# Optimization experiments

Measured on AMD Instinct MI355X. Metric: run time of the kernel, lower is better.

## Reference

```python
import jax, jax.numpy as jnp
import numpy as np

N, M = 1024, 1024
GATES = ["ii", "hi", "if", "hf", "ig", "hg", "io", "ho"]


def setup_inputs() -> dict:
    key = jax.random.key(0)
    names = ["x", "h", "c"] + [f"{p}_{g}" for g in GATES for p in ("L", "R", "b")]
    keys = jax.random.split(key, len(names))
    out = {}
    for nm, k in zip(names, keys):
        if nm in ("x", "h", "c"):
            sh = (N, M)
            scale = 1.0
        else:
            p = nm.split("_")[0]
            sh = {"L": (N, N), "R": (M, M), "b": (N, M)}[p]
            scale = 0.05  # keep gate pre-activations in a sane range
        out[nm] = jax.random.normal(k, sh, dtype=jnp.float32) * scale
    return out


def _klin(L, R, b, x):
    # kronecker_addmm: left @ x @ right + bias
    return L @ x @ R + b


def reference(x, h, c,
              L_ii, R_ii, b_ii, L_hi, R_hi, b_hi,
              L_if, R_if, b_if, L_hf, R_hf, b_hf,
              L_ig, R_ig, b_ig, L_hg, R_hg, b_hg,
              L_io, R_io, b_io, L_ho, R_ho, b_ho):
    i = jax.nn.sigmoid(_klin(L_ii, R_ii, b_ii, x) + _klin(L_hi, R_hi, b_hi, h))
    f = jax.nn.sigmoid(_klin(L_if, R_if, b_if, x) + _klin(L_hf, R_hf, b_hf, h))
    g = jnp.tanh(_klin(L_ig, R_ig, b_ig, x) + _klin(L_hg, R_hg, b_hg, h))
    o = jax.nn.sigmoid(_klin(L_io, R_io, b_io, x) + _klin(L_ho, R_ho, b_ho, h))
    c_new = f * c + i * g
    h_new = o * jnp.tanh(c_new)
    return (h_new, c_new)
```

## Files before the change

kernel.cpp:

```cpp
#include <hip/hip_runtime.h>
#include <stdint.h>

typedef __bf16 bf16x8 __attribute__((ext_vector_type(8)));
typedef float  f32x4  __attribute__((ext_vector_type(4)));
typedef uint16_t u16;

#define MAT_ELEMS (1024 * 1024)
#define LDK 1024


__device__ __forceinline__ u16 to_bf16(float f) {
  union { float f; uint32_t u; } v; v.f = f;
  uint32_t u = v.u;
  uint32_t r = u + 0x7FFFu + ((u >> 16) & 1u);
  return (u16)(r >> 16);
}

__device__ __forceinline__ float bf16_to_f32(u16 b) {
  union { uint32_t u; float f; } v; v.u = ((uint32_t)b) << 16;
  return v.f;
}

__device__ __forceinline__ void gll16(const void* g, void* l) {
  __builtin_amdgcn_global_load_lds(
      (__attribute__((address_space(1))) void*)const_cast<void*>(g),
      (__attribute__((address_space(3))) void*)(l),
      16, 0, 0);
}

__device__ __forceinline__ float fast_sigmoid(float x) {
  x = fminf(fmaxf(x, -30.f), 30.f);
  return 1.0f / (1.0f + __expf(-x));
}

__device__ __forceinline__ float fast_tanh(float x) {
  x = fminf(fmaxf(x, -15.f), 15.f);
  float e = __expf(2.0f * x);
  return (e - 1.0f) / (e + 1.0f);
}


struct P8  { const float* p[8]; };
struct P10 { const float* p[10]; };
struct B8  { const float* b[8]; };

__global__ __launch_bounds__(256) void cast8_kernel(P8 s, u16* __restrict__ dst) {
  const float* src = s.p[blockIdx.y];
  u16* d = dst + ((size_t)blockIdx.y << 20);
  int i = (blockIdx.x * 256 + threadIdx.x) * 4;
  f32x4 v = *reinterpret_cast<const f32x4*>(src + i);
  ushort4 o;
  o.x = to_bf16(v[0]); o.y = to_bf16(v[1]);
  o.z = to_bf16(v[2]); o.w = to_bf16(v[3]);
  *reinterpret_cast<ushort4*>(d + i) = o;
}

__global__ __launch_bounds__(256) void transpose_cast_kernel(P10 s, u16* __restrict__ dstbase) {
  __shared__ float tile[32][65];
  const float* src = s.p[blockIdx.z];
  u16* dst = dstbase + ((size_t)blockIdx.z << 20);
  int c0 = blockIdx.x * 64;
  int r0 = blockIdx.y * 32;
  int cl = threadIdx.x & 63;
  int rg = threadIdx.x >> 6;
#pragma unroll
  for (int i = 0; i < 8; ++i) {
    int r = rg + i * 4;
    tile[r][cl] = src[(size_t)(r0 + r) * 1024 + c0 + cl];
  }
  __syncthreads();
  int kl = threadIdx.x & 31;
  int ng = threadIdx.x >> 5;
#pragma unroll
  for (int i = 0; i < 8; ++i) {
    int n = ng + i * 8;
    dst[(size_t)(c0 + n) * 1024 + r0 + kl] = to_bf16(tile[kl][n]);
  }
}


__device__ __forceinline__ void gemm128_dbuf(
    const u16* __restrict__ A, const u16* __restrict__ B,
    int row0, int col0, u16* __restrict__ out,
    u16* As0, u16* As1, u16* Bs0, u16* Bs1)
{
  const int tid  = threadIdx.x;
  const int lane = tid & 63;
  const int w    = tid >> 6;
  const int wr   = w >> 1;
  const int wc   = w & 1;
  const int r16  = lane & 15;
  const int kg   = lane >> 4;

  f32x4 acc[4][4];
#pragma unroll
  for (int m = 0; m < 4; ++m)
#pragma unroll
    for (int n = 0; n < 4; ++n) {
      f32x4 z = {0.f, 0.f, 0.f, 0.f};
      acc[m][n] = z;
    }

  const int srow = tid >> 2;
  const int skk  = (tid & 3) * 8;

  auto stage = [&](u16* Asb, u16* Bsb, int kt) {
    const u16* Ak = A + kt * 32 + skk;
    const u16* Bk = B + kt * 32 + skk;
    gll16(Ak + (size_t)(row0 + srow)      * LDK, Asb + srow * 32 + skk);
    gll16(Ak + (size_t)(row0 + srow + 64) * LDK, Asb + (srow + 64) * 32 + skk);
    gll16(Bk + (size_t)(col0 + srow)      * LDK, Bsb + srow * 32 + skk);
    gll16(Bk + (size_t)(col0 + srow + 64) * LDK, Bsb + (srow + 64) * 32 + skk);
  };

  auto compute = [&](const u16* Asb, const u16* Bsb) {
    bf16x8 af[4], bfr[4];
#pragma unroll
    for (int m = 0; m < 4; ++m)
      af[m] = *reinterpret_cast<const bf16x8*>(Asb + (wr * 64 + m * 16 + r16) * 32 + kg * 8);
#pragma unroll
    for (int n = 0; n < 4; ++n)
      bfr[n] = *reinterpret_cast<const bf16x8*>(Bsb + (wc * 64 + n * 16 + r16) * 32 + kg * 8);
#pragma unroll
    for (int m = 0; m < 4; ++m)
#pragma unroll
      for (int n = 0; n < 4; ++n)
        acc[m][n] = __builtin_amdgcn_mfma_f32_16x16x32_bf16(af[m], bfr[n], acc[m][n], 0, 0, 0);
  };

  stage(As0, Bs0, 0);
  __syncthreads();

  for (int kt = 0; kt < 32; kt += 2) {
    stage(As1, Bs1, kt + 1);
    compute(As0, Bs0);
    __syncthreads();
    if (kt + 2 < 32) stage(As0, Bs0, kt + 2);
    compute(As1, Bs1);
    __syncthreads();
  }

#pragma unroll
  for (int m = 0; m < 4; ++m) {
#pragma unroll
    for (int r = 0; r < 4; ++r) {
      int row = row0 + wr * 64 + m * 16 + kg * 4 + r;
#pragma unroll
      for (int n = 0; n < 4; ++n) {
        int col = col0 + wc * 64 + n * 16 + r16;
        out[(size_t)row * 1024 + col] = to_bf16(acc[m][n][r]);
      }
    }
  }
}

__device__ __forceinline__ void swz_decode(int bx, int& g, int& row0, int& col0) {
  int wg = ((bx & 7) << 6) | (bx >> 3);
  g = wg >> 6;
  int tile = wg & 63;
  row0 = (tile >> 3) * 128;
  col0 = (tile & 7) * 128;
}

__global__ __launch_bounds__(256) void gemm_stage1_kernel(
    const u16* __restrict__ Lb, const u16* __restrict__ xT,
    const u16* __restrict__ hT, u16* __restrict__ Tbuf)
{
  __shared__ u16 As0[128 * 32], As1[128 * 32];
  __shared__ u16 Bs0[128 * 32], Bs1[128 * 32];
  int g, row0, col0;
  swz_decode(blockIdx.x, g, row0, col0);
  const u16* A = Lb + ((size_t)g << 20);
  const u16* B = (g & 1) ? hT : xT;
  gemm128_dbuf(A, B, row0, col0, Tbuf + ((size_t)g << 20), As0, As1, Bs0, Bs1);
}

__global__ __launch_bounds__(256) void gemm_stage2_kernel(
    const u16* __restrict__ Tbuf, const u16* __restrict__ RT,
    u16* __restrict__ P)
{
  __shared__ u16 As0[128 * 32], As1[128 * 32];
  __shared__ u16 Bs0[128 * 32], Bs1[128 * 32];
  int g, row0, col0;
  swz_decode(blockIdx.x, g, row0, col0);
  const u16* A = Tbuf + ((size_t)g << 20);
  const u16* B = RT   + ((size_t)g << 20);
  gemm128_dbuf(A, B, row0, col0, P + ((size_t)g << 20), As0, As1, Bs0, Bs1);
}

__global__ __launch_bounds__(256) void lstm_cell_kernel(
    const u16* __restrict__ P, B8 bp, const float* __restrict__ c,
    float* __restrict__ out)
{
  int i = (blockIdx.x * 256 + threadIdx.x) * 4;
  ushort4 pv[8];
#pragma unroll
  for (int g = 0; g < 8; ++g)
    pv[g] = *reinterpret_cast<const ushort4*>(P + (size_t)g * MAT_ELEMS + i);
  f32x4 bv[8];
#pragma unroll
  for (int g = 0; g < 8; ++g)
    bv[g] = *reinterpret_cast<const f32x4*>(bp.b[g] + i);
  f32x4 cc = *reinterpret_cast<const f32x4*>(c + i);
  f32x4 hn, cn;
#pragma unroll
  for (int j = 0; j < 4; ++j) {
    float pi = bf16_to_f32((&pv[0].x)[j]) + bf16_to_f32((&pv[1].x)[j]) + bv[0][j] + bv[1][j];
    float pf = bf16_to_f32((&pv[2].x)[j]) + bf16_to_f32((&pv[3].x)[j]) + bv[2][j] + bv[3][j];
    float pg = bf16_to_f32((&pv[4].x)[j]) + bf16_to_f32((&pv[5].x)[j]) + bv[4][j] + bv[5][j];
    float po = bf16_to_f32((&pv[6].x)[j]) + bf16_to_f32((&pv[7].x)[j]) + bv[6][j] + bv[7][j];
    float ig = fast_sigmoid(pi);
    float fg = fast_sigmoid(pf);
    float gg = fast_tanh(pg);
    float og = fast_sigmoid(po);
    float cv = fg * cc[j] + ig * gg;
    cn[j] = cv;
    hn[j] = og * fast_tanh(cv);
  }
  *reinterpret_cast<f32x4*>(out + i) = hn;
  *reinterpret_cast<f32x4*>(out + MAT_ELEMS + i) = cn;
}


extern "C" void kernel_launch(void* const* d_in, const int* in_sizes, int n_in,
                              void* d_out, int out_size, void* d_ws, size_t ws_size,
                              hipStream_t stream) {
  const float* x = (const float*)d_in[0];
  const float* h = (const float*)d_in[1];
  const float* c = (const float*)d_in[2];

  u16* Lb   = (u16*)d_ws;
  u16* xT   = Lb + ((size_t)8 << 20);
  u16* hT   = xT + ((size_t)1 << 20);
  u16* RT   = hT + ((size_t)1 << 20);
  u16* Tbuf = RT + ((size_t)8 << 20);
  u16* P    = Tbuf + ((size_t)8 << 20);

  P8 lp;
  for (int g = 0; g < 8; ++g) lp.p[g] = (const float*)d_in[3 + 3 * g];
  P10 tp;
  tp.p[0] = x; tp.p[1] = h;
  for (int g = 0; g < 8; ++g) tp.p[2 + g] = (const float*)d_in[4 + 3 * g];
  B8 bp;
  for (int g = 0; g < 8; ++g) bp.b[g] = (const float*)d_in[5 + 3 * g];

  cast8_kernel<<<dim3(1024, 8), 256, 0, stream>>>(lp, Lb);
  transpose_cast_kernel<<<dim3(16, 32, 10), 256, 0, stream>>>(tp, xT);
  gemm_stage1_kernel<<<512, 256, 0, stream>>>(Lb, xT, hT, Tbuf);
  gemm_stage2_kernel<<<512, 256, 0, stream>>>(Tbuf, RT, P);
  lstm_cell_kernel<<<1024, 256, 0, stream>>>(P, bp, c, (float*)d_out);
}
```

Baseline: 232.2 us.

## Use 128x256 GEMM tiles with 8 waves, swizzled LDS and explicit vmcnt barriers

Both bf16 GEMM stages move from 128x128 tiles with 4 waves to 128x256 tiles with 8 waves (2x4 wave grid). The grid drops to 256 blocks, so each block reuses its A tile across twice as many output columns. LDS staging now XOR-swizzles the 16-byte k-chunks by row, which is meant to reduce bank conflicts on the fragment reads. __syncthreads is replaced by an explicit vmcnt(0) wait, an s_barrier and a sched_barrier, so the async global-to-LDS loads are known to be complete before the buffer is read. The trade-off is roughly one block per CU with fewer independent workgroups to hide latency, and a larger LDS footprint per block.

```diff
diff --git a/kernel.cpp b/kernel.cpp
--- a/kernel.cpp
+++ b/kernel.cpp
@@ -26,6 +26,12 @@
       (__attribute__((address_space(1))) void*)const_cast<void*>(g),
       (__attribute__((address_space(3))) void*)(l),
       16, 0, 0);
+}
+
+__device__ __forceinline__ void wait_barrier() {
+  asm volatile("s_waitcnt vmcnt(0)" ::: "memory");
+  __builtin_amdgcn_s_barrier();
+  __builtin_amdgcn_sched_barrier(0);
 }
 
 __device__ __forceinline__ float fast_sigmoid(float x) {
@@ -79,18 +85,57 @@
 }
 
 
-__device__ __forceinline__ void gemm128_dbuf(
+struct GemmCtx {
+  const u16* A; const u16* B;
+  int row0, col0;
+  int tid, wr, wc, r16, kg, sw;
+};
+
+__device__ __forceinline__ void stage_tile(const GemmCtx& c, u16* As, u16* Bs, int kt) {
+  int rho = c.tid >> 2;
+  int sig = c.tid & 3;
+  int swc = (sig ^ ((c.tid >> 3) & 3)) * 8;
+  int kcol = kt * 32 + swc;
+  gll16(c.A + (size_t)(c.row0 + rho) * LDK + kcol, As + c.tid * 8);
+  gll16(c.B + (size_t)(c.col0 + rho) * LDK + kcol, Bs + c.tid * 8);
+  gll16(c.B + (size_t)(c.col0 + rho + 128) * LDK + kcol, Bs + c.tid * 8 + 4096);
+}
+
+__device__ __forceinline__ void compute_tile(const GemmCtx& c, const u16* As,
+                                             const u16* Bs, f32x4 acc[4][4]) {
+  bf16x8 af[4], bfr[4];
+#pragma unroll
+  for (int n = 0; n < 4; ++n) {
+    int Rb = c.wc * 64 + n * 16 + c.r16;
+    bfr[n] = *reinterpret_cast<const bf16x8*>(Bs + Rb * 32 + ((c.kg ^ c.sw) * 8));
+  }
+#pragma unroll
+  for (int m = 0; m < 4; ++m) {
+    int Ra = c.wr * 64 + m * 16 + c.r16;
+    af[m] = *reinterpret_cast<const bf16x8*>(As + Ra * 32 + ((c.kg ^ c.sw) * 8));
+  }
+#pragma unroll
+  for (int m = 0; m < 4; ++m)
+#pragma unroll
+    for (int n = 0; n < 4; ++n)
+      acc[m][n] = __builtin_amdgcn_mfma_f32_16x16x32_bf16(af[m], bfr[n], acc[m][n], 0, 0, 0);
+}
+
+__device__ __forceinline__ void gemm_body(
     const u16* __restrict__ A, const u16* __restrict__ B,
     int row0, int col0, u16* __restrict__ out,
-    u16* As0, u16* As1, u16* Bs0, u16* Bs1)
-{
-  const int tid  = threadIdx.x;
-  const int lane = tid & 63;
-  const int w    = tid >> 6;
-  const int wr   = w >> 1;
-  const int wc   = w & 1;
-  const int r16  = lane & 15;
-  const int kg   = lane >> 4;
+    u16* As0, u16* Bs0, u16* As1, u16* Bs1)
+{
+  GemmCtx c;
+  c.A = A; c.B = B; c.row0 = row0; c.col0 = col0;
+  c.tid = threadIdx.x;
+  int lane = c.tid & 63;
+  int w = c.tid >> 6;
+  c.wr  = w >> 2;
+  c.wc  = w & 3;
+  c.r16 = lane & 15;
+  c.kg  = lane >> 4;
+  c.sw  = (c.r16 >> 1) & 3;
 
   f32x4 acc[4][4];
 #pragma unroll
@@ -101,53 +146,26 @@
       acc[m][n] = z;
     }
 
-  const int srow = tid >> 2;
-  const int skk  = (tid & 3) * 8;
-
-  auto stage = [&](u16* Asb, u16* Bsb, int kt) {
-    const u16* Ak = A + kt * 32 + skk;
-    const u16* Bk = B + kt * 32 + skk;
-    gll16(Ak + (size_t)(row0 + srow)      * LDK, Asb + srow * 32 + skk);
-    gll16(Ak + (size_t)(row0 + srow + 64) * LDK, Asb + (srow + 64) * 32 + skk);
-    gll16(Bk + (size_t)(col0 + srow)      * LDK, Bsb + srow * 32 + skk);
-    gll16(Bk + (size_t)(col0 + srow + 64) * LDK, Bsb + (srow + 64) * 32 + skk);
-  };
-
-  auto compute = [&](const u16* Asb, const u16* Bsb) {
-    bf16x8 af[4], bfr[4];
-#pragma unroll
-    for (int m = 0; m < 4; ++m)
-      af[m] = *reinterpret_cast<const bf16x8*>(Asb + (wr * 64 + m * 16 + r16) * 32 + kg * 8);
-#pragma unroll
-    for (int n = 0; n < 4; ++n)
-      bfr[n] = *reinterpret_cast<const bf16x8*>(Bsb + (wc * 64 + n * 16 + r16) * 32 + kg * 8);
-#pragma unroll
-    for (int m = 0; m < 4; ++m)
-#pragma unroll
-      for (int n = 0; n < 4; ++n)
-        acc[m][n] = __builtin_amdgcn_mfma_f32_16x16x32_bf16(af[m], bfr[n], acc[m][n], 0, 0, 0);
-  };
-
-  stage(As0, Bs0, 0);
-  __syncthreads();
+  stage_tile(c, As0, Bs0, 0);
+  wait_barrier();
 
   for (int kt = 0; kt < 32; kt += 2) {
-    stage(As1, Bs1, kt + 1);
-    compute(As0, Bs0);
-    __syncthreads();
-    if (kt + 2 < 32) stage(As0, Bs0, kt + 2);
-    compute(As1, Bs1);
-    __syncthreads();
+    stage_tile(c, As1, Bs1, kt + 1);
+    compute_tile(c, As0, Bs0, acc);
+    wait_barrier();
+    if (kt + 2 < 32) stage_tile(c, As0, Bs0, kt + 2);
+    compute_tile(c, As1, Bs1, acc);
+    wait_barrier();
   }
 
 #pragma unroll
   for (int m = 0; m < 4; ++m) {
 #pragma unroll
     for (int r = 0; r < 4; ++r) {
-      int row = row0 + wr * 64 + m * 16 + kg * 4 + r;
+      int row = row0 + c.wr * 64 + m * 16 + c.kg * 4 + r;
 #pragma unroll
       for (int n = 0; n < 4; ++n) {
-        int col = col0 + wc * 64 + n * 16 + r16;
+        int col = col0 + c.wc * 64 + n * 16 + c.r16;
         out[(size_t)row * 1024 + col] = to_bf16(acc[m][n][r]);
       }
     }
@@ -155,37 +173,37 @@
 }
 
 __device__ __forceinline__ void swz_decode(int bx, int& g, int& row0, int& col0) {
-  int wg = ((bx & 7) << 6) | (bx >> 3);
-  g = wg >> 6;
-  int tile = wg & 63;
-  row0 = (tile >> 3) * 128;
-  col0 = (tile & 7) * 128;
-}
-
-__global__ __launch_bounds__(256) void gemm_stage1_kernel(
+  int wg = ((bx & 7) << 5) | (bx >> 3);
+  g = wg >> 5;
+  int t = wg & 31;
+  row0 = (t >> 2) * 128;
+  col0 = (t & 3) * 256;
+}
+
+__global__ __launch_bounds__(512) void gemm_stage1_kernel(
     const u16* __restrict__ Lb, const u16* __restrict__ xT,
     const u16* __restrict__ hT, u16* __restrict__ Tbuf)
 {
-  __shared__ u16 As0[128 * 32], As1[128 * 32];
-  __shared__ u16 Bs0[128 * 32], Bs1[128 * 32];
+  __shared__ u16 As0[128 * 32], Bs0[256 * 32];
+  __shared__ u16 As1[128 * 32], Bs1[256 * 32];
   int g, row0, col0;
   swz_decode(blockIdx.x, g, row0, col0);
   const u16* A = Lb + ((size_t)g << 20);
   const u16* B = (g & 1) ? hT : xT;
-  gemm128_dbuf(A, B, row0, col0, Tbuf + ((size_t)g << 20), As0, As1, Bs0, Bs1);
-}
-
-__global__ __launch_bounds__(256) void gemm_stage2_kernel(
+  gemm_body(A, B, row0, col0, Tbuf + ((size_t)g << 20), As0, Bs0, As1, Bs1);
+}
+
+__global__ __launch_bounds__(512) void gemm_stage2_kernel(
     const u16* __restrict__ Tbuf, const u16* __restrict__ RT,
     u16* __restrict__ P)
 {
-  __shared__ u16 As0[128 * 32], As1[128 * 32];
-  __shared__ u16 Bs0[128 * 32], Bs1[128 * 32];
+  __shared__ u16 As0[128 * 32], Bs0[256 * 32];
+  __shared__ u16 As1[128 * 32], Bs1[256 * 32];
   int g, row0, col0;
   swz_decode(blockIdx.x, g, row0, col0);
   const u16* A = Tbuf + ((size_t)g << 20);
   const u16* B = RT   + ((size_t)g << 20);
-  gemm128_dbuf(A, B, row0, col0, P + ((size_t)g << 20), As0, As1, Bs0, Bs1);
+  gemm_body(A, B, row0, col0, P + ((size_t)g << 20), As0, Bs0, As1, Bs1);
 }
 
 __global__ __launch_bounds__(256) void lstm_cell_kernel(
@@ -246,7 +264,7 @@
 
   cast8_kernel<<<dim3(1024, 8), 256, 0, stream>>>(lp, Lb);
   transpose_cast_kernel<<<dim3(16, 32, 10), 256, 0, stream>>>(tp, xT);
-  gemm_stage1_kernel<<<512, 256, 0, stream>>>(Lb, xT, hT, Tbuf);
-  gemm_stage2_kernel<<<512, 256, 0, stream>>>(Tbuf, RT, P);
+  gemm_stage1_kernel<<<256, 512, 0, stream>>>(Lb, xT, hT, Tbuf);
+  gemm_stage2_kernel<<<256, 512, 0, stream>>>(Tbuf, RT, P);
   lstm_cell_kernel<<<1024, 256, 0, stream>>>(P, bp, c, (float*)d_out);
 }
```

Result: slower. 242.3 us (+4.4%).

## Replace 128x128 GEMM with 256x256 eight-wave pipelined tile kernel

Applied to the files above, without the earlier changes.

The two batched GEMM stages move from 128x128 tiles (256 threads, BK=32) to 256x256 tiles with 512 threads, BK=64 and 128 KB of dynamic LDS. The new kernel uses an XOR-swizzled LDS layout and splits each k-tile into four phases that interleave global-to-LDS loads with MFMA bursts under explicit barriers, s_setprio and vmcnt waits. The aim is more data reuse per tile, fewer LDS bank conflicts and loads overlapped with compute. The cost is only 128 workgroups on a 256-CU device, so about half the CUs sit idle, plus high register and LDS pressure.

```diff
diff --git a/kernel.cpp b/kernel.cpp
--- a/kernel.cpp
+++ b/kernel.cpp
@@ -6,7 +6,6 @@
 typedef uint16_t u16;
 
 #define MAT_ELEMS (1024 * 1024)
-#define LDK 1024
 
 
 __device__ __forceinline__ u16 to_bf16(float f) {
@@ -26,6 +25,11 @@
       (__attribute__((address_space(1))) void*)const_cast<void*>(g),
       (__attribute__((address_space(3))) void*)(l),
       16, 0, 0);
+}
+
+__device__ __forceinline__ void barrier_pin() {
+  __builtin_amdgcn_s_barrier();
+  __builtin_amdgcn_sched_barrier(0);
 }
 
 __device__ __forceinline__ float fast_sigmoid(float x) {
@@ -79,113 +83,204 @@
 }
 
 
-__device__ __forceinline__ void gemm128_dbuf(
-    const u16* __restrict__ A, const u16* __restrict__ B,
-    int row0, int col0, u16* __restrict__ out,
-    u16* As0, u16* As1, u16* Bs0, u16* Bs1)
+#define HALF_U16 8192
+#define BUF_U16  16384
+
+__device__ __forceinline__ void stage_half(const u16* __restrict__ src,
+                                           u16* __restrict__ dst, int tid) {
+#pragma unroll
+  for (int s = 0; s < 2; ++s) {
+    int idx = s * 512 + tid;
+    int row = idx >> 3;
+    int gs  = (idx & 7) ^ (row & 7);
+    gll16(src + (size_t)row * 1024 + gs * 8, dst + idx * 8);
+  }
+}
+
+__device__ void gemm8p(const u16* __restrict__ A, const u16* __restrict__ B,
+                       int row0, int col0, u16* __restrict__ out, u16* smem)
 {
   const int tid  = threadIdx.x;
   const int lane = tid & 63;
   const int w    = tid >> 6;
-  const int wr   = w >> 1;
-  const int wc   = w & 1;
+  const int wm   = w >> 2;
+  const int wn   = w & 3;
+  const int wh   = wn >> 1;
   const int r16  = lane & 15;
   const int kg   = lane >> 4;
-
-  f32x4 acc[4][4];
-#pragma unroll
-  for (int m = 0; m < 4; ++m)
+  const int rsw  = r16 & 7;
+  const int brow = (wn & 1) * 64;
+
+  u16* Abuf = smem;
+  u16* Bbuf = smem + 2 * BUF_U16;
+
+  u16* A0w = Abuf + wm * HALF_U16;
+  u16* A1w = Abuf + BUF_U16 + wm * HALF_U16;
+  u16* B0w = Bbuf + wh * HALF_U16;
+  u16* B1w = Bbuf + BUF_U16 + wh * HALF_U16;
+
+  u16* A0d0 = Abuf;            u16* A0d1 = Abuf + HALF_U16;
+  u16* A1d0 = Abuf + BUF_U16;  u16* A1d1 = Abuf + BUF_U16 + HALF_U16;
+  u16* B0d0 = Bbuf;            u16* B0d1 = Bbuf + HALF_U16;
+  u16* B1d0 = Bbuf + BUF_U16;  u16* B1d1 = Bbuf + BUF_U16 + HALF_U16;
+
+  auto asrc = [&](int kt, int h) { return A + (size_t)(row0 + h * 128) * 1024 + kt * 64; };
+  auto bsrc = [&](int kt, int h) { return B + (size_t)(col0 + h * 128) * 1024 + kt * 64; };
+
+  f32x4 acc[8][4];
+#pragma unroll
+  for (int m = 0; m < 8; ++m)
 #pragma unroll
     for (int n = 0; n < 4; ++n) {
       f32x4 z = {0.f, 0.f, 0.f, 0.f};
       acc[m][n] = z;
     }
 
-  const int srow = tid >> 2;
-  const int skk  = (tid & 3) * 8;
-
-  auto stage = [&](u16* Asb, u16* Bsb, int kt) {
-    const u16* Ak = A + kt * 32 + skk;
-    const u16* Bk = B + kt * 32 + skk;
-    gll16(Ak + (size_t)(row0 + srow)      * LDK, Asb + srow * 32 + skk);
-    gll16(Ak + (size_t)(row0 + srow + 64) * LDK, Asb + (srow + 64) * 32 + skk);
-    gll16(Bk + (size_t)(col0 + srow)      * LDK, Bsb + srow * 32 + skk);
-    gll16(Bk + (size_t)(col0 + srow + 64) * LDK, Bsb + (srow + 64) * 32 + skk);
+  stage_half(asrc(0, 0), A0d0, tid); stage_half(asrc(0, 1), A0d1, tid);
+  stage_half(bsrc(0, 0), B0d0, tid); stage_half(bsrc(0, 1), B0d1, tid);
+  stage_half(bsrc(1, 0), B1d0, tid); stage_half(bsrc(1, 1), B1d1, tid);
+  asm volatile("s_waitcnt vmcnt(4)" ::: "memory");
+  barrier_pin();
+
+  auto rf = [&](const u16* hb, int rowin, int ks) {
+    int slot = (ks * 4 + kg) ^ rsw;
+    return *reinterpret_cast<const bf16x8*>(hb + rowin * 64 + slot * 8);
   };
 
-  auto compute = [&](const u16* Asb, const u16* Bsb) {
-    bf16x8 af[4], bfr[4];
-#pragma unroll
-    for (int m = 0; m < 4; ++m)
-      af[m] = *reinterpret_cast<const bf16x8*>(Asb + (wr * 64 + m * 16 + r16) * 32 + kg * 8);
-#pragma unroll
-    for (int n = 0; n < 4; ++n)
-      bfr[n] = *reinterpret_cast<const bf16x8*>(Bsb + (wc * 64 + n * 16 + r16) * 32 + kg * 8);
-#pragma unroll
-    for (int m = 0; m < 4; ++m)
-#pragma unroll
-      for (int n = 0; n < 4; ++n)
-        acc[m][n] = __builtin_amdgcn_mfma_f32_16x16x32_bf16(af[m], bfr[n], acc[m][n], 0, 0, 0);
+  auto tile = [&](const u16* Ac, const u16* Bc,
+                  u16* Ad0, u16* Ad1, u16* Bd0, u16* Bd1,
+                  const u16* As0, const u16* As1,
+                  const u16* Bs0, const u16* Bs1,
+                  bool g1, bool g2, bool vm4)
+  {
+    bf16x8 aq[4][2], b01[2][2], b23[2][2];
+#pragma unroll
+    for (int mf = 0; mf < 4; ++mf) {
+      aq[mf][0] = rf(Ac, mf * 16 + r16, 0);
+      aq[mf][1] = rf(Ac, mf * 16 + r16, 1);
+    }
+#pragma unroll
+    for (int nf = 0; nf < 2; ++nf) {
+      b01[nf][0] = rf(Bc, brow + nf * 16 + r16, 0);
+      b01[nf][1] = rf(Bc, brow + nf * 16 + r16, 1);
+    }
+    if (g1) stage_half(As0, Ad0, tid);
+    barrier_pin();
+    __builtin_amdgcn_s_setprio(1);
+#pragma unroll
+    for (int mf = 0; mf < 4; ++mf)
+#pragma unroll
+      for (int nf = 0; nf < 2; ++nf)
+#pragma unroll
+        for (int ks = 0; ks < 2; ++ks)
+          acc[mf][nf] = __builtin_amdgcn_mfma_f32_16x16x32_bf16(aq[mf][ks], b01[nf][ks], acc[mf][nf], 0, 0, 0);
+    __builtin_amdgcn_s_setprio(0);
+    barrier_pin();
+#pragma unroll
+    for (int nf = 0; nf < 2; ++nf) {
+      b23[nf][0] = rf(Bc, brow + (nf + 2) * 16 + r16, 0);
+      b23[nf][1] = rf(Bc, brow + (nf + 2) * 16 + r16, 1);
+    }
+    if (g1) stage_half(As1, Ad1, tid);
+    barrier_pin();
+    __builtin_amdgcn_s_setprio(1);
+#pragma unroll
+    for (int mf = 0; mf < 4; ++mf)
+#pragma unroll
+      for (int nf = 0; nf < 2; ++nf)
+#pragma unroll
+        for (int ks = 0; ks < 2; ++ks)
+          acc[mf][2 + nf] = __builtin_amdgcn_mfma_f32_16x16x32_bf16(aq[mf][ks], b23[nf][ks], acc[mf][2 + nf], 0, 0, 0);
+    __builtin_amdgcn_s_setprio(0);
+    barrier_pin();
+#pragma unroll
+    for (int mf = 0; mf < 4; ++mf) {
+      aq[mf][0] = rf(Ac, 64 + mf * 16 + r16, 0);
+      aq[mf][1] = rf(Ac, 64 + mf * 16 + r16, 1);
+    }
+    if (g2) stage_half(Bs0, Bd0, tid);
+    barrier_pin();
+    __builtin_amdgcn_s_setprio(1);
+#pragma unroll
+    for (int mf = 0; mf < 4; ++mf)
+#pragma unroll
+      for (int nf = 0; nf < 2; ++nf)
+#pragma unroll
+        for (int ks = 0; ks < 2; ++ks)
+          acc[4 + mf][nf] = __builtin_amdgcn_mfma_f32_16x16x32_bf16(aq[mf][ks], b01[nf][ks], acc[4 + mf][nf], 0, 0, 0);
+    __builtin_amdgcn_s_setprio(0);
+    barrier_pin();
+    if (g2) stage_half(Bs1, Bd1, tid);
+    if (vm4) asm volatile("s_waitcnt vmcnt(4)" ::: "memory");
+    else     asm volatile("s_waitcnt vmcnt(0)" ::: "memory");
+    barrier_pin();
+    __builtin_amdgcn_s_setprio(1);
+#pragma unroll
+    for (int mf = 0; mf < 4; ++mf)
+#pragma unroll
+      for (int nf = 0; nf < 2; ++nf)
+#pragma unroll
+        for (int ks = 0; ks < 2; ++ks)
+          acc[4 + mf][2 + nf] = __builtin_amdgcn_mfma_f32_16x16x32_bf16(aq[mf][ks], b23[nf][ks], acc[4 + mf][2 + nf], 0, 0, 0);
+    __builtin_amdgcn_s_setprio(0);
+    barrier_pin();
   };
 
-  stage(As0, Bs0, 0);
-  __syncthreads();
-
-  for (int kt = 0; kt < 32; kt += 2) {
-    stage(As1, Bs1, kt + 1);
-    compute(As0, Bs0);
-    __syncthreads();
-    if (kt + 2 < 32) stage(As0, Bs0, kt + 2);
-    compute(As1, Bs1);
-    __syncthreads();
-  }
-
-#pragma unroll
-  for (int m = 0; m < 4; ++m) {
+  for (int i = 0; i < 8; ++i) {
+    int kt = 2 * i;
+    bool nl = (i < 7);
+    tile(A0w, B0w, A1d0, A1d1, B0d0, B0d1,
+         asrc(kt + 1, 0), asrc(kt + 1, 1), bsrc(kt + 2, 0), bsrc(kt + 2, 1),
+         true, nl, nl);
+    tile(A1w, B1w, A0d0, A0d1, B1d0, B1d1,
+         asrc(kt + 2, 0), asrc(kt + 2, 1), bsrc(kt + 3, 0), bsrc(kt + 3, 1),
+         nl, nl, nl);
+  }
+
+#pragma unroll
+  for (int mf = 0; mf < 8; ++mf) {
 #pragma unroll
     for (int r = 0; r < 4; ++r) {
-      int row = row0 + wr * 64 + m * 16 + kg * 4 + r;
-#pragma unroll
-      for (int n = 0; n < 4; ++n) {
-        int col = col0 + wc * 64 + n * 16 + r16;
-        out[(size_t)row * 1024 + col] = to_bf16(acc[m][n][r]);
+      int row = row0 + wm * 128 + mf * 16 + kg * 4 + r;
+#pragma unroll
+      for (int nf = 0; nf < 4; ++nf) {
+        int col = col0 + wn * 64 + nf * 16 + r16;
+        out[(size_t)row * 1024 + col] = to_bf16(acc[mf][nf][r]);
       }
     }
   }
 }
 
 __device__ __forceinline__ void swz_decode(int bx, int& g, int& row0, int& col0) {
-  int wg = ((bx & 7) << 6) | (bx >> 3);
-  g = wg >> 6;
-  int tile = wg & 63;
-  row0 = (tile >> 3) * 128;
-  col0 = (tile & 7) * 128;
-}
-
-__global__ __launch_bounds__(256) void gemm_stage1_kernel(
+  int wg = ((bx & 7) << 4) | (bx >> 3);
+  g = wg >> 4;
+  int t = wg & 15;
+  row0 = (t >> 2) * 256;
+  col0 = (t & 3) * 256;
+}
+
+__global__ __launch_bounds__(512, 2) void gemm_stage1_kernel(
     const u16* __restrict__ Lb, const u16* __restrict__ xT,
     const u16* __restrict__ hT, u16* __restrict__ Tbuf)
 {
-  __shared__ u16 As0[128 * 32], As1[128 * 32];
-  __shared__ u16 Bs0[128 * 32], Bs1[128 * 32];
+  extern __shared__ u16 smem[];
   int g, row0, col0;
   swz_decode(blockIdx.x, g, row0, col0);
   const u16* A = Lb + ((size_t)g << 20);
   const u16* B = (g & 1) ? hT : xT;
-  gemm128_dbuf(A, B, row0, col0, Tbuf + ((size_t)g << 20), As0, As1, Bs0, Bs1);
-}
-
-__global__ __launch_bounds__(256) void gemm_stage2_kernel(
+  gemm8p(A, B, row0, col0, Tbuf + ((size_t)g << 20), smem);
+}
+
+__global__ __launch_bounds__(512, 2) void gemm_stage2_kernel(
     const u16* __restrict__ Tbuf, const u16* __restrict__ RT,
     u16* __restrict__ P)
 {
-  __shared__ u16 As0[128 * 32], As1[128 * 32];
-  __shared__ u16 Bs0[128 * 32], Bs1[128 * 32];
+  extern __shared__ u16 smem[];
   int g, row0, col0;
   swz_decode(blockIdx.x, g, row0, col0);
   const u16* A = Tbuf + ((size_t)g << 20);
-  const u16* B = RT   + ((size_t)g << 20);
-  gemm128_dbuf(A, B, row0, col0, P + ((size_t)g << 20), As0, As1, Bs0, Bs1);
+  const u16* B = RT + ((size_t)g << 20);
+  gemm8p(A, B, row0, col0, P + ((size_t)g << 20), smem);
 }
 
 __global__ __launch_bounds__(256) void lstm_cell_kernel(
@@ -246,7 +341,7 @@
 
   cast8_kernel<<<dim3(1024, 8), 256, 0, stream>>>(lp, Lb);
   transpose_cast_kernel<<<dim3(16, 32, 10), 256, 0, stream>>>(tp, xT);
-  gemm_stage1_kernel<<<512, 256, 0, stream>>>(Lb, xT, hT, Tbuf);
-  gemm_stage2_kernel<<<512, 256, 0, stream>>>(Tbuf, RT, P);
+  gemm_stage1_kernel<<<128, 512, 131072, stream>>>(Lb, xT, hT, Tbuf);
+  gemm_stage2_kernel<<<128, 512, 131072, stream>>>(Tbuf, RT, P);
   lstm_cell_kernel<<<1024, 256, 0, stream>>>(P, bp, c, (float*)d_out);
 }
```

New measurement: 258.2 us. 1.11x slower.
